# Kernel tuning notes

Hardware: AMD Instinct MI355X
Metric: run time of the kernel (lower is better)

## Reference

```python
import jax, jax.numpy as jnp
import numpy as np

B, H, N, C = 1024, 768, 100000, 42
LABELED_WEIGHT = 0.7
NUM_LABELED = 100000  # used verbatim in (1 - num_labeled) per the original source
EPS = 1e-8  # F.cosine_similarity default eps


def setup_inputs() -> dict:
    key = jax.random.key(0)
    k1, k2, k3, k4 = jax.random.split(key, 4)
    return {
        "weak_data": jax.random.normal(k1, (B, H), dtype=jnp.float32),
        "weak_logits": jax.random.normal(k2, (B, C), dtype=jnp.float32),
        "labeled_memory": jax.random.normal(k3, (N, H), dtype=jnp.float32),
        "labeled_logits": jax.random.normal(k4, (N, C), dtype=jnp.float32),
    }


def reference(weak_data, weak_logits, labeled_memory, labeled_logits):
    # cosine similarity: normalize rows with eps-clamped norms, then one GEMM
    dn = weak_data / jnp.maximum(jnp.linalg.norm(weak_data, axis=-1, keepdims=True), EPS)
    mn = labeled_memory / jnp.maximum(jnp.linalg.norm(labeled_memory, axis=-1, keepdims=True), EPS)
    sim = jnp.einsum("bh,nh->bn", dn, mn)  # [B, N] similarity (the large intermediate)
    ids = jnp.argmax(sim, axis=1)          # 1-NN index per batch row
    batch_logits = labeled_logits[ids]     # gather [B, C]
    # faithful to source: coefficient is (1 - num_labeled), as written in update_logits
    return batch_logits * LABELED_WEIGHT + (1.0 - NUM_LABELED) * weak_logits
```

## Files before the change

kernel.cpp:

```cpp
#include <hip/hip_runtime.h>
#include <stdint.h>

#define B_ROWS 1024
#define H_DIM  768
#define N_ROWS 100000
#define C_DIM  42
#define NB     64
#define NCHUNK ((N_ROWS + NB - 1) / NB)
#define K2_BLOCKS 782
#define K2_THREADS 512

typedef __attribute__((ext_vector_type(8))) short short8;
typedef __attribute__((ext_vector_type(4))) float f32x4;

__device__ __forceinline__ unsigned short f2bf(float f) {
    union { float f; unsigned u; } x; x.f = f;
    unsigned r = x.u + 0x7FFFu + ((x.u >> 16) & 1u);
    return (unsigned short)(r >> 16);
}

__device__ __forceinline__ unsigned long long packvi(float v, unsigned n) {
    unsigned u = __float_as_uint(v);
    u = (u & 0x80000000u) ? ~u : (u | 0x80000000u);
    return ((unsigned long long)u << 32) | (unsigned long long)(~n);
}

__global__ void k_convA(const float* __restrict__ wd, unsigned short* __restrict__ A) {
    int idx = blockIdx.x * 256 + threadIdx.x;
    float4 v = reinterpret_cast<const float4*>(wd)[idx];
    union { unsigned short s[4]; uint2 u; } o;
    o.s[0] = f2bf(v.x); o.s[1] = f2bf(v.y); o.s[2] = f2bf(v.z); o.s[3] = f2bf(v.w);
    reinterpret_cast<uint2*>(A)[idx] = o.u;
}

__global__ __launch_bounds__(512, 2) void k_simmax(
    const float* __restrict__ mem,
    const unsigned short* __restrict__ A,
    unsigned long long* __restrict__ partial)
{
    __shared__ __align__(16) char ldsB[NB * 1536];
    __shared__ float ldsN[NB];

    const int t    = threadIdx.x;
    const int lane = t & 63;
    const int wv   = t >> 6;
    const int fr   = lane & 15;
    const int kgrp = lane >> 4;

    for (int ci = 0; ci < 2; ++ci) {
        const int c = blockIdx.x + ci * K2_BLOCKS;
        if (c >= NCHUNK) break;
        if (ci) __syncthreads();

        {
            const int r  = t >> 3;
            const int cb = (t & 7) * 4;
            const int n  = c * NB + r;
            const bool valid = (n < N_ROWS);
            const float* src = mem + (long long)n * H_DIM + cb;
            char* dst = ldsB + r * 1536;
            const int sw = (r & 7) << 4;
            float ss = 0.f;
            #pragma unroll
            for (int i = 0; i < 24; ++i) {
                float4 v;
                if (valid) v = *reinterpret_cast<const float4*>(src + i * 32);
                else       v = make_float4(0.f, 0.f, 0.f, 0.f);
                ss += v.x*v.x + v.y*v.y + v.z*v.z + v.w*v.w;
                union { unsigned short s[4]; uint2 u; } o;
                o.s[0]=f2bf(v.x); o.s[1]=f2bf(v.y); o.s[2]=f2bf(v.z); o.s[3]=f2bf(v.w);
                int off = (cb + i * 32) * 2;
                *reinterpret_cast<uint2*>(dst + (off ^ sw)) = o.u;
            }
            ss += __shfl_xor(ss, 1);
            ss += __shfl_xor(ss, 2);
            ss += __shfl_xor(ss, 4);
            if ((t & 7) == 0)
                ldsN[r] = valid ? (1.0f / fmaxf(sqrtf(ss), 1e-8f)) : 0.0f;
        }
        __syncthreads();

        float invn[4];
        #pragma unroll
        for (int nt = 0; nt < 4; ++nt) invn[nt] = ldsN[nt * 16 + fr];

        #pragma unroll
        for (int gi = 0; gi < 2; ++gi) {
            const int b0 = (wv + 8 * gi) * 64;
            f32x4 acc[4][4];
            #pragma unroll
            for (int m = 0; m < 4; ++m)
                #pragma unroll
                for (int n = 0; n < 4; ++n)
                    acc[m][n] = (f32x4){0.f, 0.f, 0.f, 0.f};

            #pragma unroll 4
            for (int k = 0; k < 24; ++k) {
                const int k0 = k * 32 + kgrp * 8;
                short8 af[4], bf[4];
                #pragma unroll
                for (int m = 0; m < 4; ++m) {
                    const unsigned short* ap = A + (b0 + m * 16 + fr) * H_DIM + k0;
                    af[m] = *reinterpret_cast<const short8*>(ap);
                }
                #pragma unroll
                for (int n = 0; n < 4; ++n) {
                    int roww = n * 16 + fr;
                    int off  = roww * 1536 + k0 * 2;
                    off ^= (roww & 7) << 4;
                    bf[n] = *reinterpret_cast<const short8*>(ldsB + off);
                }
                #pragma unroll
                for (int m = 0; m < 4; ++m)
                    #pragma unroll
                    for (int n = 0; n < 4; ++n)
                        acc[m][n] = __builtin_amdgcn_mfma_f32_16x16x32_bf16(af[m], bf[n], acc[m][n], 0, 0, 0);
            }

            #pragma unroll
            for (int m = 0; m < 4; ++m) {
                #pragma unroll
                for (int r = 0; r < 4; ++r) {
                    unsigned long long best = 0ull;
                    #pragma unroll
                    for (int nt = 0; nt < 4; ++nt) {
                        unsigned nglob = (unsigned)(c * NB + nt * 16 + fr);
                        float v = acc[m][nt][r] * invn[nt];
                        unsigned long long p = (nglob < N_ROWS) ? packvi(v, nglob) : 0ull;
                        best = (p > best) ? p : best;
                    }
                    #pragma unroll
                    for (int s = 1; s < 16; s <<= 1) {
                        unsigned long long o = __shfl_xor(best, s);
                        best = (o > best) ? o : best;
                    }
                    if (fr == 0) {
                        int brow = b0 + m * 16 + kgrp * 4 + r;
                        partial[(long long)c * 1024 + brow] = best;
                    }
                }
            }
        }
    }
}

__global__ void k_final(const unsigned long long* __restrict__ partial,
                        const float* __restrict__ wlog,
                        const float* __restrict__ llog,
                        float* __restrict__ out)
{
    __shared__ unsigned long long red[16][17];
    __shared__ int sidx[16];
    const int t  = threadIdx.x;
    const int b0 = blockIdx.x * 16;
    const int i  = t >> 4, j = t & 15;

    unsigned long long best = 0ull;
    for (int c = j; c < NCHUNK; c += 16) {
        unsigned long long p = partial[(long long)c * 1024 + b0 + i];
        best = (p > best) ? p : best;
    }
    red[i][j] = best;
    __syncthreads();
    if (t < 16) {
        unsigned long long m = red[t][0];
        #pragma unroll
        for (int jj = 1; jj < 16; ++jj) { unsigned long long p = red[t][jj]; m = (p > m) ? p : m; }
        sidx[t] = (int)(~(unsigned)(m & 0xFFFFFFFFull));
    }
    __syncthreads();
    for (int e = t; e < 16 * C_DIM; e += 256) {
        int bi = e / C_DIM, cc = e % C_DIM;
        int b  = b0 + bi;
        out[b * C_DIM + cc] = 0.7f * llog[(long long)sidx[bi] * C_DIM + cc]
                            - 99999.0f * wlog[b * C_DIM + cc];
    }
}

extern "C" void kernel_launch(void* const* d_in, const int* in_sizes, int n_in,
                              void* d_out, int out_size, void* d_ws, size_t ws_size,
                              hipStream_t stream) {
    const float* weak_data   = (const float*)d_in[0];
    const float* weak_logits = (const float*)d_in[1];
    const float* mem         = (const float*)d_in[2];
    const float* llog        = (const float*)d_in[3];
    float* out = (float*)d_out;

    unsigned short*     A       = (unsigned short*)d_ws;
    unsigned long long* partial = (unsigned long long*)((char*)d_ws + (2u << 20));

    k_convA <<<768, 256, 0, stream>>>(weak_data, A);
    k_simmax<<<K2_BLOCKS, K2_THREADS, 0, stream>>>(mem, A, partial);
    k_final <<<64, 256, 0, stream>>>(partial, weak_logits, llog, out);
}
```

Baseline: 922.8 us.

## Rewrite similarity argmax with FP8 MFMA, register-resident A, double-buffered memory tiles

Switches the similarity GEMM from bf16 to fp8 MFMA, preloads the weak-data fragments into registers per wave, and splits the grid into 8 batch-row groups times 64 persistent column partitions. Each partition streams 32-row memory chunks through a double-buffered LDS stage with LDS atomic norm accumulation and keeps running per-row argmax in registers. The final reduction collapses to a 64-way wave shuffle. The aim is to cut conversion and GEMM cost and to overlap loading with compute, but fp8 precision may flip near-tie argmax results, and each memory chunk is now read eight times (once per batch-row group).

Result: no change. 922.7 us (-0.0%).

```diff
diff --git a/kernel.cpp b/kernel.cpp
--- a/kernel.cpp
+++ b/kernel.cpp
@@ -5,176 +5,185 @@
 #define H_DIM  768
 #define N_ROWS 100000
 #define C_DIM  42
-#define NB     64
-#define NCHUNK ((N_ROWS + NB - 1) / NB)
-#define K2_BLOCKS 782
-#define K2_THREADS 512
-
-typedef __attribute__((ext_vector_type(8))) short short8;
+#define NB     32
+#define NCHUNK 3125
+#define NP     64
+#define NY     8
+
 typedef __attribute__((ext_vector_type(4))) float f32x4;
-
-__device__ __forceinline__ unsigned short f2bf(float f) {
-    union { float f; unsigned u; } x; x.f = f;
-    unsigned r = x.u + 0x7FFFu + ((x.u >> 16) & 1u);
-    return (unsigned short)(r >> 16);
-}
-
-__device__ __forceinline__ unsigned long long packvi(float v, unsigned n) {
+typedef unsigned long long ull;
+
+__device__ __forceinline__ ull packvi(float v, unsigned n) {
     unsigned u = __float_as_uint(v);
     u = (u & 0x80000000u) ? ~u : (u | 0x80000000u);
-    return ((unsigned long long)u << 32) | (unsigned long long)(~n);
-}
-
-__global__ void k_convA(const float* __restrict__ wd, unsigned short* __restrict__ A) {
-    int idx = blockIdx.x * 256 + threadIdx.x;
-    float4 v = reinterpret_cast<const float4*>(wd)[idx];
-    union { unsigned short s[4]; uint2 u; } o;
-    o.s[0] = f2bf(v.x); o.s[1] = f2bf(v.y); o.s[2] = f2bf(v.z); o.s[3] = f2bf(v.w);
-    reinterpret_cast<uint2*>(A)[idx] = o.u;
-}
-
-__global__ __launch_bounds__(512, 2) void k_simmax(
+    return ((ull)u << 32) | (ull)(~n);
+}
+
+__device__ __forceinline__ int pk8(float4 v) {
+    int d = __builtin_amdgcn_cvt_pk_fp8_f32(v.x, v.y, 0, false);
+    d     = __builtin_amdgcn_cvt_pk_fp8_f32(v.z, v.w, d, true);
+    return d;
+}
+
+__device__ __forceinline__ int swz(int k, int kg, int n) {
+    return (k * 1024 + kg * 256 + n * 8) ^ ((kg << 3) | ((k & 3) << 5));
+}
+
+__global__ void k_convA(const float* __restrict__ wd, int2* __restrict__ A2) {
+    int g = blockIdx.x * 256 + threadIdx.x;
+    int row = g / 96;
+    int rem = g - row * 96;
+    int k = rem >> 2, kgrp = rem & 3;
+    const float* s = wd + row * H_DIM + k * 32 + kgrp * 8;
+    float4 v0 = *reinterpret_cast<const float4*>(s);
+    float4 v1 = *reinterpret_cast<const float4*>(s + 4);
+    int rg = row >> 4, fr = row & 15;
+    A2[((rg * 24 + k) * 64 + kgrp * 16 + fr)] = make_int2(pk8(v0), pk8(v1));
+}
+
+__global__ __launch_bounds__(256, 2) void k_simmax(
     const float* __restrict__ mem,
-    const unsigned short* __restrict__ A,
-    unsigned long long* __restrict__ partial)
+    const long* __restrict__ A2,
+    ull* __restrict__ partial)
 {
-    __shared__ __align__(16) char ldsB[NB * 1536];
-    __shared__ float ldsN[NB];
+    __shared__ __align__(16) char ldsB[2][24 * 1024];
+    __shared__ float ldsS[4][NB];
 
     const int t    = threadIdx.x;
     const int lane = t & 63;
     const int wv   = t >> 6;
     const int fr   = lane & 15;
     const int kgrp = lane >> 4;
-
-    for (int ci = 0; ci < 2; ++ci) {
-        const int c = blockIdx.x + ci * K2_BLOCKS;
-        if (c >= NCHUNK) break;
-        if (ci) __syncthreads();
-
-        {
-            const int r  = t >> 3;
-            const int cb = (t & 7) * 4;
-            const int n  = c * NB + r;
-            const bool valid = (n < N_ROWS);
-            const float* src = mem + (long long)n * H_DIM + cb;
-            char* dst = ldsB + r * 1536;
-            const int sw = (r & 7) << 4;
-            float ss = 0.f;
-            #pragma unroll
-            for (int i = 0; i < 24; ++i) {
-                float4 v;
-                if (valid) v = *reinterpret_cast<const float4*>(src + i * 32);
-                else       v = make_float4(0.f, 0.f, 0.f, 0.f);
-                ss += v.x*v.x + v.y*v.y + v.z*v.z + v.w*v.w;
-                union { unsigned short s[4]; uint2 u; } o;
-                o.s[0]=f2bf(v.x); o.s[1]=f2bf(v.y); o.s[2]=f2bf(v.z); o.s[3]=f2bf(v.w);
-                int off = (cb + i * 32) * 2;
-                *reinterpret_cast<uint2*>(dst + (off ^ sw)) = o.u;
-            }
-            ss += __shfl_xor(ss, 1);
-            ss += __shfl_xor(ss, 2);
-            ss += __shfl_xor(ss, 4);
-            if ((t & 7) == 0)
-                ldsN[r] = valid ? (1.0f / fmaxf(sqrtf(ss), 1e-8f)) : 0.0f;
+    const int bx   = blockIdx.x;
+    const int y    = bx >> 6;
+    const int p    = bx & 63;
+
+    const int RG0 = y * 8 + wv * 2;
+    long Afr[2][24];
+    #pragma unroll
+    for (int rg = 0; rg < 2; ++rg) {
+        const long* ap = A2 + (size_t)(RG0 + rg) * 24 * 64 + lane;
+        #pragma unroll
+        for (int k = 0; k < 24; ++k) Afr[rg][k] = ap[k * 64];
+    }
+
+    float    bv[2][2][4];
+    unsigned bi[2][2][4];
+    #pragma unroll
+    for (int rg = 0; rg < 2; ++rg)
+        #pragma unroll
+        for (int nt = 0; nt < 2; ++nt)
+            #pragma unroll
+            for (int r = 0; r < 4; ++r) { bv[rg][nt][r] = -1e30f; bi[rg][nt][r] = 0u; }
+
+    const int nc = (p < 53) ? 49 : 48;
+
+    auto stage = [&](int c, int bb, int ns) {
+        #pragma unroll 4
+        for (int uu = 0; uu < 12; ++uu) {
+            int ug = t + 256 * uu;
+            int n  = ug / 96;
+            int rm = ug - n * 96;
+            int k = rm >> 2, kg = rm & 3;
+            const float* s = mem + (size_t)(c * NB + n) * H_DIM + k * 32 + kg * 8;
+            float4 v0 = *reinterpret_cast<const float4*>(s);
+            float4 v1 = *reinterpret_cast<const float4*>(s + 4);
+            float ss = v0.x*v0.x + v0.y*v0.y + v0.z*v0.z + v0.w*v0.w
+                     + v1.x*v1.x + v1.y*v1.y + v1.z*v1.z + v1.w*v1.w;
+            atomicAdd(&ldsS[ns][n], ss);
+            *reinterpret_cast<int2*>(&ldsB[bb][swz(k, kg, n)]) =
+                make_int2(pk8(v0), pk8(v1));
         }
+    };
+
+    if (t < NB) { ldsS[0][t] = 0.f; ldsS[1][t] = 0.f; }
+    __syncthreads();
+    stage(p, 0, 0);
+
+    for (int i = 0; i < nc; ++i) {
         __syncthreads();
-
-        float invn[4];
-        #pragma unroll
-        for (int nt = 0; nt < 4; ++nt) invn[nt] = ldsN[nt * 16 + fr];
-
-        #pragma unroll
-        for (int gi = 0; gi < 2; ++gi) {
-            const int b0 = (wv + 8 * gi) * 64;
-            f32x4 acc[4][4];
-            #pragma unroll
-            for (int m = 0; m < 4; ++m)
-                #pragma unroll
-                for (int n = 0; n < 4; ++n)
-                    acc[m][n] = (f32x4){0.f, 0.f, 0.f, 0.f};
-
-            #pragma unroll 4
-            for (int k = 0; k < 24; ++k) {
-                const int k0 = k * 32 + kgrp * 8;
-                short8 af[4], bf[4];
-                #pragma unroll
-                for (int m = 0; m < 4; ++m) {
-                    const unsigned short* ap = A + (b0 + m * 16 + fr) * H_DIM + k0;
-                    af[m] = *reinterpret_cast<const short8*>(ap);
-                }
-                #pragma unroll
-                for (int n = 0; n < 4; ++n) {
-                    int roww = n * 16 + fr;
-                    int off  = roww * 1536 + k0 * 2;
-                    off ^= (roww & 7) << 4;
-                    bf[n] = *reinterpret_cast<const short8*>(ldsB + off);
-                }
-                #pragma unroll
-                for (int m = 0; m < 4; ++m)
-                    #pragma unroll
-                    for (int n = 0; n < 4; ++n)
-                        acc[m][n] = __builtin_amdgcn_mfma_f32_16x16x32_bf16(af[m], bf[n], acc[m][n], 0, 0, 0);
-            }
-
-            #pragma unroll
-            for (int m = 0; m < 4; ++m) {
-                #pragma unroll
-                for (int r = 0; r < 4; ++r) {
-                    unsigned long long best = 0ull;
-                    #pragma unroll
-                    for (int nt = 0; nt < 4; ++nt) {
-                        unsigned nglob = (unsigned)(c * NB + nt * 16 + fr);
-                        float v = acc[m][nt][r] * invn[nt];
-                        unsigned long long p = (nglob < N_ROWS) ? packvi(v, nglob) : 0ull;
-                        best = (p > best) ? p : best;
-                    }
-                    #pragma unroll
-                    for (int s = 1; s < 16; s <<= 1) {
-                        unsigned long long o = __shfl_xor(best, s);
-                        best = (o > best) ? o : best;
-                    }
-                    if (fr == 0) {
-                        int brow = b0 + m * 16 + kgrp * 4 + r;
-                        partial[(long long)c * 1024 + brow] = best;
-                    }
-                }
+        if (t < NB) ldsS[(i + 2) & 3][t] = 0.f;
+        if (i + 1 < nc) stage(p + (i + 1) * NP, (i + 1) & 1, (i + 1) & 3);
+
+        const int c  = p + i * NP;
+        const int bb = i & 1;
+        const int ns = i & 3;
+
+        f32x4 acc[2][2];
+        #pragma unroll
+        for (int rg = 0; rg < 2; ++rg)
+            #pragma unroll
+            for (int nt = 0; nt < 2; ++nt)
+                acc[rg][nt] = (f32x4){0.f, 0.f, 0.f, 0.f};
+
+        #pragma unroll
+        for (int k = 0; k < 24; ++k) {
+            long bfr0 = *reinterpret_cast<const long*>(&ldsB[bb][swz(k, kgrp, fr)]);
+            long bfr1 = *reinterpret_cast<const long*>(&ldsB[bb][swz(k, kgrp, 16 + fr)]);
+            #pragma unroll
+            for (int rg = 0; rg < 2; ++rg) {
+                acc[rg][0] = __builtin_amdgcn_mfma_f32_16x16x32_fp8_fp8(Afr[rg][k], bfr0, acc[rg][0], 0, 0, 0);
+                acc[rg][1] = __builtin_amdgcn_mfma_f32_16x16x32_fp8_fp8(Afr[rg][k], bfr1, acc[rg][1], 0, 0, 0);
             }
         }
+
+        float inv0 = __frsqrt_rn(fmaxf(ldsS[ns][fr],      1e-16f));
+        float inv1 = __frsqrt_rn(fmaxf(ldsS[ns][16 + fr], 1e-16f));
+        const unsigned n0 = (unsigned)(c * NB) + (unsigned)fr;
+        #pragma unroll
+        for (int rg = 0; rg < 2; ++rg)
+            #pragma unroll
+            for (int r = 0; r < 4; ++r) {
+                float v0 = acc[rg][0][r] * inv0;
+                float v1 = acc[rg][1][r] * inv1;
+                bool p0 = v0 > bv[rg][0][r];
+                bv[rg][0][r] = p0 ? v0 : bv[rg][0][r];
+                bi[rg][0][r] = p0 ? n0 : bi[rg][0][r];
+                bool p1 = v1 > bv[rg][1][r];
+                bv[rg][1][r] = p1 ? v1 : bv[rg][1][r];
+                bi[rg][1][r] = p1 ? (n0 + 16) : bi[rg][1][r];
+            }
     }
-}
-
-__global__ void k_final(const unsigned long long* __restrict__ partial,
+
+    #pragma unroll
+    for (int rg = 0; rg < 2; ++rg)
+        #pragma unroll
+        for (int r = 0; r < 4; ++r) {
+            ull P0 = packvi(bv[rg][0][r], bi[rg][0][r]);
+            ull P1 = packvi(bv[rg][1][r], bi[rg][1][r]);
+            ull P  = (P1 > P0) ? P1 : P0;
+            #pragma unroll
+            for (int s = 1; s < 16; s <<= 1) {
+                ull o = __shfl_xor(P, s);
+                P = (o > P) ? o : P;
+            }
+            if (fr == 0) {
+                int b = y * 128 + wv * 32 + rg * 16 + kgrp * 4 + r;
+                partial[(size_t)p * B_ROWS + b] = P;
+            }
+        }
+}
+
+__global__ void k_final(const ull* __restrict__ partial,
                         const float* __restrict__ wlog,
                         const float* __restrict__ llog,
                         float* __restrict__ out)
 {
-    __shared__ unsigned long long red[16][17];
-    __shared__ int sidx[16];
-    const int t  = threadIdx.x;
-    const int b0 = blockIdx.x * 16;
-    const int i  = t >> 4, j = t & 15;
-
-    unsigned long long best = 0ull;
-    for (int c = j; c < NCHUNK; c += 16) {
-        unsigned long long p = partial[(long long)c * 1024 + b0 + i];
-        best = (p > best) ? p : best;
+    const int t    = threadIdx.x;
+    const int lane = t & 63;
+    const int wv   = t >> 6;
+    const int b    = blockIdx.x * 4 + wv;
+
+    ull P = partial[(size_t)lane * B_ROWS + b];
+    #pragma unroll
+    for (int s = 1; s < 64; s <<= 1) {
+        ull o = __shfl_xor(P, s);
+        P = (o > P) ? o : P;
     }
-    red[i][j] = best;
-    __syncthreads();
-    if (t < 16) {
-        unsigned long long m = red[t][0];
-        #pragma unroll
-        for (int jj = 1; jj < 16; ++jj) { unsigned long long p = red[t][jj]; m = (p > m) ? p : m; }
-        sidx[t] = (int)(~(unsigned)(m & 0xFFFFFFFFull));
-    }
-    __syncthreads();
-    for (int e = t; e < 16 * C_DIM; e += 256) {
-        int bi = e / C_DIM, cc = e % C_DIM;
-        int b  = b0 + bi;
-        out[b * C_DIM + cc] = 0.7f * llog[(long long)sidx[bi] * C_DIM + cc]
-                            - 99999.0f * wlog[b * C_DIM + cc];
-    }
+    int idx = (int)(~(unsigned)(P & 0xFFFFFFFFull));
+    if (lane < C_DIM)
+        out[b * C_DIM + lane] = 0.7f * llog[(size_t)idx * C_DIM + lane]
+                              - 99999.0f * wlog[b * C_DIM + lane];
 }
 
 extern "C" void kernel_launch(void* const* d_in, const int* in_sizes, int n_in,
@@ -186,10 +195,10 @@
     const float* llog        = (const float*)d_in[3];
     float* out = (float*)d_out;
 
-    unsigned short*     A       = (unsigned short*)d_ws;
-    unsigned long long* partial = (unsigned long long*)((char*)d_ws + (2u << 20));
-
-    k_convA <<<768, 256, 0, stream>>>(weak_data, A);
-    k_simmax<<<K2_BLOCKS, K2_THREADS, 0, stream>>>(mem, A, partial);
-    k_final <<<64, 256, 0, stream>>>(partial, weak_logits, llog, out);
-}
+    int2* A2      = (int2*)d_ws;
+    ull*  partial = (ull*)((char*)d_ws + 0x100000);
+
+    k_convA <<<384, 256, 0, stream>>>(weak_data, A2);
+    k_simmax<<<NY * NP, 256, 0, stream>>>(mem, (const long*)A2, partial);
+    k_final <<<256, 256, 0, stream>>>(partial, weak_logits, llog, out);
+}
```
